# Kernel optimization log

Hardware: AMD Instinct MI355X
Metric: run time of the kernel (lower is better)

The kernel has to match this reference:

```python
import jax, jax.numpy as jnp
import numpy as np

NUM_EXPERTS = 8


def setup_inputs() -> dict:
    key = jax.random.key(0)
    k1, k2 = jax.random.split(key)
    G, T, D, E = 4, 2048, 1024, NUM_EXPERTS
    token_inputs = jax.random.normal(k1, (G, T, D), dtype=jnp.float32)
    router_weight = jax.random.normal(k2, (E, D), dtype=jnp.float32) * 0.02
    router_bias = jnp.zeros((E,), dtype=jnp.float32)
    return {
        "token_inputs": token_inputs,
        "router_weight": router_weight,
        "router_bias": router_bias,
        "expert_capacity": 320,
    }


def _routing(probs, expert_capacities):
    """Experts-preferred assignment: experts pick tokens in order, each up to
    its capacity, from tokens not yet taken by earlier experts."""
    G, T, E = probs.shape
    max_cap = max(expert_capacities)
    dispatch = jnp.zeros((G, T, E, max_cap), dtype=jnp.int32)
    combine = jnp.zeros((G, T, E, max_cap), dtype=probs.dtype)
    available = jnp.ones((G, T), dtype=probs.dtype)  # 1 if token unassigned
    g_idx = jnp.arange(G)[:, None]
    for e, cap in enumerate(expert_capacities):  # static small loop over experts
        masked = probs[:, :, e] * available                 # [G, T]
        gate, idx = jax.lax.top_k(masked, cap)              # [G, cap]
        c_idx = jnp.arange(cap)[None, :]
        dispatch = dispatch.at[g_idx, idx, e, c_idx].set(1)
        combine = combine.at[g_idx, idx, e, c_idx].set(gate)
        available = available.at[g_idx, idx].set(0.0)       # chosen tokens now taken
    return dispatch, combine


def reference(token_inputs, router_weight, router_bias, expert_capacity):
    x = token_inputs.astype(jnp.float32)
    # router logits: [G, T, E]
    logits = jnp.einsum("gtd,ed->gte", x, router_weight) + router_bias
    probs = jax.nn.softmax(logits, axis=-1)
    capacities = [int(expert_capacity)] * NUM_EXPERTS
    dispatch_mask, combine_array = _routing(probs, capacities)
    # router z-loss: mean over groups*tokens of logsumexp(logits)^2
    log_z = jax.nn.logsumexp(logits, axis=-1)
    z_loss = jnp.sum(log_z ** 2) / (logits.shape[0] * logits.shape[1])
    auxiliary_loss = jnp.float32(0.0)
    router_causal_loss = jnp.float32(0.0)
    return dispatch_mask, combine_array, auxiliary_loss, z_loss, router_causal_loss
```

## Files before the change

kernel.cpp:

```cpp
#include <hip/hip_runtime.h>

#define NEXP 8
typedef unsigned long long u64;
typedef unsigned int u32;

__global__ __launch_bounds__(512) void probs_fill_kernel(
    const float* __restrict__ x,
    const float* __restrict__ w,
    const float* __restrict__ bias,
    float* __restrict__ probsT,
    double* __restrict__ zpart,
    float* __restrict__ out,
    long long nout4,
    long long GT, int npb, int nfb)
{
    if ((int)blockIdx.x >= npb) {
        const int fb = (int)blockIdx.x - npb;
        const long long stride = (long long)nfb * 512;
        const float4 z = make_float4(0.f, 0.f, 0.f, 0.f);
        for (long long k = (long long)fb * 512 + threadIdx.x; k < nout4; k += stride) {
            reinterpret_cast<float4*>(out)[k] = z;
        }
        return;
    }

    __shared__ float wl[NEXP * 1024];
    __shared__ double zred[8];
    for (int i = threadIdx.x; i < NEXP * 1024 / 4; i += 512) {
        reinterpret_cast<float4*>(wl)[i] = reinterpret_cast<const float4*>(w)[i];
    }
    __syncthreads();

    const int wave = threadIdx.x >> 6;
    const int lane = threadIdx.x & 63;
    const long long t = (long long)blockIdx.x * 8 + wave;
    const float* xr = x + t * 1024;

    float acc[NEXP];
#pragma unroll
    for (int e = 0; e < NEXP; ++e) acc[e] = 0.f;

#pragma unroll
    for (int c = 0; c < 4; ++c) {
        const int d = c * 256 + lane * 4;
        const float4 xv = *reinterpret_cast<const float4*>(xr + d);
#pragma unroll
        for (int e = 0; e < NEXP; ++e) {
            const float4 wv = *reinterpret_cast<const float4*>(wl + e * 1024 + d);
            acc[e] = fmaf(xv.x, wv.x, acc[e]);
            acc[e] = fmaf(xv.y, wv.y, acc[e]);
            acc[e] = fmaf(xv.z, wv.z, acc[e]);
            acc[e] = fmaf(xv.w, wv.w, acc[e]);
        }
    }
#pragma unroll
    for (int e = 0; e < NEXP; ++e) {
#pragma unroll
        for (int off = 32; off; off >>= 1) acc[e] += __shfl_xor(acc[e], off, 64);
    }

    if (lane == 0) {
        double l[NEXP];
        double mx = -1e300;
#pragma unroll
        for (int e = 0; e < NEXP; ++e) {
            l[e] = (double)acc[e] + (double)bias[e];
            mx = fmax(mx, l[e]);
        }
        double ex[NEXP];
        double s = 0.0;
#pragma unroll
        for (int e = 0; e < NEXP; ++e) { ex[e] = exp(l[e] - mx); s += ex[e]; }
        const double inv = 1.0 / s;
#pragma unroll
        for (int e = 0; e < NEXP; ++e) probsT[(long long)e * GT + t] = (float)(ex[e] * inv);
        const double lse = mx + log(s);
        zred[wave] = lse * lse;
    }
    __syncthreads();
    if (threadIdx.x == 0) {
        double s = 0.0;
#pragma unroll
        for (int i = 0; i < 8; ++i) s += zred[i];
        zpart[blockIdx.x] = s;
    }
}

__global__ __launch_bounds__(256) void ranksort_kernel(
    const float* __restrict__ probsT,
    u64* __restrict__ skey,
    int T, int G, long long GT)
{
    __shared__ u64 keys[2048];
    const int nsub = T / 256;
    const int pair = blockIdx.x / nsub;
    const int sub  = blockIdx.x % nsub;
    const int e = pair / G;
    const int g = pair % G;
    const float* p = probsT + (long long)e * GT + (long long)g * T;

    for (int j = threadIdx.x; j < T; j += 256) {
        keys[j] = ((u64)__float_as_uint(p[j]) << 32) | (u32)(~(u32)j);
    }
    __syncthreads();

    const int i = sub * 256 + threadIdx.x;
    const u64 ki = keys[i];
    int r = 0;
    const ulonglong2* k2 = reinterpret_cast<const ulonglong2*>(keys);
#pragma unroll 8
    for (int j = 0; j < T / 2; ++j) {
        const ulonglong2 q = k2[j];
        r += (q.x > ki);
        r += (q.y > ki);
    }
    skey[(long long)pair * T + r] = ki;
}

__global__ __launch_bounds__(1024) void assign_kernel(
    const u64* __restrict__ skey,
    const double* __restrict__ zpart,
    int nzpart,
    float* __restrict__ out,
    int T, int G, int cap, long long GT)
{
    const int g = blockIdx.x;
    const int tid = threadIdx.x;
    const int lane = tid & 63;
    const int w = tid >> 6;

    __shared__ int avail[2048];
    __shared__ int cnt[32];
    __shared__ int off[32];
    __shared__ int totS;

    avail[tid] = 1;
    avail[tid + 1024] = 1;

    float* dispatch = out;
    float* combine  = out + GT * (long long)NEXP * cap;
    const long long gbase = (long long)g * T;
    const u64 lmask = (lane == 0) ? 0ull : ((~0ull) >> (64 - lane));

    for (int e = 0; e < NEXP; ++e) {
        __syncthreads();
        const long long kb = (long long)(e * G + g) * T;
        const u64 k0 = skey[kb + tid];
        const u64 k1 = skey[kb + tid + 1024];
        const u32 idx0 = ~(u32)k0;
        const u32 idx1 = ~(u32)k1;
        const float v0 = __uint_as_float((u32)(k0 >> 32));
        const float v1 = __uint_as_float((u32)(k1 >> 32));
        const int f0 = avail[idx0];
        const int f1 = avail[idx1];
        const u64 m0 = __ballot(f0);
        const u64 m1 = __ballot(f1);
        if (lane == 0) { cnt[w] = __popcll(m0); cnt[16 + w] = __popcll(m1); }
        __syncthreads();
        if (w == 0) {
            int v = (lane < 32) ? cnt[lane] : 0;
#pragma unroll
            for (int o = 1; o < 32; o <<= 1) { int t2 = __shfl_up(v, o, 64); if (lane >= o) v += t2; }
            if (lane < 32) off[lane] = v - cnt[lane];
            if (lane == 31) totS = v;
        }
        __syncthreads();
        const int S = totS;
        const int pre0 = off[w] + __popcll(m0 & lmask);
        const int pre1 = off[16 + w] + __popcll(m1 & lmask);
        const bool s0 = f0 && pre0 < cap;
        const bool s1 = f1 && pre1 < cap;
        if (s0) {
            const long long o_ = ((gbase + idx0) * NEXP + e) * (long long)cap + pre0;
            dispatch[o_] = 1.0f;
            combine[o_]  = v0;
        }
        if (s1) {
            const long long o_ = ((gbase + idx1) * NEXP + e) * (long long)cap + pre1;
            dispatch[o_] = 1.0f;
            combine[o_]  = v1;
        }
        if (S < cap) {
            const int u0 = 1 - avail[tid];
            const int u1 = 1 - avail[tid + 1024];
            const u64 n0 = __ballot(u0);
            const u64 n1 = __ballot(u1);
            if (lane == 0) { cnt[w] = __popcll(n0); cnt[16 + w] = __popcll(n1); }
            __syncthreads();
            if (w == 0) {
                int v = (lane < 32) ? cnt[lane] : 0;
#pragma unroll
                for (int o = 1; o < 32; o <<= 1) { int t2 = __shfl_up(v, o, 64); if (lane >= o) v += t2; }
                if (lane < 32) off[lane] = v - cnt[lane];
            }
            __syncthreads();
            const int q0 = off[w] + __popcll(n0 & lmask);
            const int q1 = off[16 + w] + __popcll(n1 & lmask);
            const int nfill = cap - S;
            if (u0 && q0 < nfill) {
                const long long o_ = ((gbase + tid) * NEXP + e) * (long long)cap + S + q0;
                dispatch[o_] = 1.0f;
            }
            if (u1 && q1 < nfill) {
                const long long o_ = ((gbase + tid + 1024) * NEXP + e) * (long long)cap + S + q1;
                dispatch[o_] = 1.0f;
            }
            __syncthreads();
        }
        if (s0) avail[idx0] = 0;
        if (s1) avail[idx1] = 0;
    }

    if (g == 0 && tid < 64) {
        double s = 0.0;
        for (int i = tid; i < nzpart; i += 64) s += zpart[i];
#pragma unroll
        for (int o = 32; o; o >>= 1) {
            s += __shfl_xor(s, o, 64);
        }
        if (tid == 0) {
            float* sc = out + 2 * GT * (long long)NEXP * cap;
            sc[0] = 0.0f;
            sc[1] = (float)(s / (double)GT);
            sc[2] = 0.0f;
        }
    }
}

extern "C" void kernel_launch(void* const* d_in, const int* in_sizes, int n_in,
                              void* d_out, int out_size, void* d_ws, size_t ws_size,
                              hipStream_t stream) {
    (void)n_in; (void)ws_size;
    const float* x    = (const float*)d_in[0];
    const float* w    = (const float*)d_in[1];
    const float* bias = (const float*)d_in[2];

    const int E = in_sizes[2];
    const int D = in_sizes[1] / E;
    const long long GT = (long long)in_sizes[0] / D;
    const int T = 2048;
    const int G = (int)(GT / T);
    const int cap = (int)(((long long)out_size - 3) / (2 * GT * E));
    const int npb = (int)(GT / 8);
    const int nfb = 2048;

    double* zpart = (double*)d_ws;
    float* probsT = (float*)((char*)d_ws + 16384);
    u64*   skey   = (u64*)((char*)d_ws + 16384 + (size_t)E * GT * sizeof(float));

    const long long nout4 = ((long long)out_size - 3) >> 2;

    probs_fill_kernel<<<npb + nfb, 512, 0, stream>>>(
        x, w, bias, probsT, zpart, (float*)d_out, nout4, GT, npb, nfb);

    ranksort_kernel<<<E * G * (T / 256), 256, 0, stream>>>(probsT, skey, T, G, GT);

    assign_kernel<<<G, 1024, 0, stream>>>(skey, zpart, npb, (float*)d_out, T, G, cap, GT);
}
```

Before: 80.13 us.

## Fuse router, rank sort and assignment into one persistent kernel with grid barriers

Merges the three kernels (probs+zero fill, rank sort, assignment) into a single 256-block persistent kernel that uses atomic-counter grid barriers between phases. Each block now handles 32 tokens, and the rank sort splits the comparison over 4 thread groups with a shared-memory reduction. The assignment phase preloads all sorted keys into registers and replaces the shared-memory prefix scans with per-wave shuffle scans, dropping several syncthreads per expert. The goal is to remove launch gaps and inter-kernel drains. In exchange it relies on all 256 blocks being co-resident and on a memset of the barrier counters, and runs fewer blocks for the zero fill and the projection.

```diff
diff --git a/kernel.cpp b/kernel.cpp
--- a/kernel.cpp
+++ b/kernel.cpp
@@ -1,141 +1,156 @@
 #include <hip/hip_runtime.h>
 
 #define NEXP 8
+#define NBLK 256
+#define NTHR 1024
+
 typedef unsigned long long u64;
 typedef unsigned int u32;
 
-__global__ __launch_bounds__(512) void probs_fill_kernel(
+union __align__(16) Smem {
+    struct { float wl[NEXP * 1024]; double zred[16]; } a;
+    struct { u64 keys[2048]; int part[NTHR]; } b;
+    struct { int avail[2048]; int cnt[32]; int cnt2[32]; } c;
+};
+
+__global__ __launch_bounds__(NTHR, 4) void moe_router_kernel(
     const float* __restrict__ x,
     const float* __restrict__ w,
     const float* __restrict__ bias,
+    float* __restrict__ out,
     float* __restrict__ probsT,
+    u64* __restrict__ skey,
     double* __restrict__ zpart,
-    float* __restrict__ out,
-    long long nout4,
-    long long GT, int npb, int nfb)
+    int* __restrict__ bar,
+    long long nout4, long long GT, int T, int G, int cap)
 {
-    if ((int)blockIdx.x >= npb) {
-        const int fb = (int)blockIdx.x - npb;
-        const long long stride = (long long)nfb * 512;
-        const float4 z = make_float4(0.f, 0.f, 0.f, 0.f);
-        for (long long k = (long long)fb * 512 + threadIdx.x; k < nout4; k += stride) {
-            reinterpret_cast<float4*>(out)[k] = z;
-        }
-        return;
-    }
-
-    __shared__ float wl[NEXP * 1024];
-    __shared__ double zred[8];
-    for (int i = threadIdx.x; i < NEXP * 1024 / 4; i += 512) {
-        reinterpret_cast<float4*>(wl)[i] = reinterpret_cast<const float4*>(w)[i];
-    }
-    __syncthreads();
-
-    const int wave = threadIdx.x >> 6;
-    const int lane = threadIdx.x & 63;
-    const long long t = (long long)blockIdx.x * 8 + wave;
-    const float* xr = x + t * 1024;
-
-    float acc[NEXP];
-#pragma unroll
-    for (int e = 0; e < NEXP; ++e) acc[e] = 0.f;
-
-#pragma unroll
-    for (int c = 0; c < 4; ++c) {
-        const int d = c * 256 + lane * 4;
-        const float4 xv = *reinterpret_cast<const float4*>(xr + d);
-#pragma unroll
-        for (int e = 0; e < NEXP; ++e) {
-            const float4 wv = *reinterpret_cast<const float4*>(wl + e * 1024 + d);
-            acc[e] = fmaf(xv.x, wv.x, acc[e]);
-            acc[e] = fmaf(xv.y, wv.y, acc[e]);
-            acc[e] = fmaf(xv.z, wv.z, acc[e]);
-            acc[e] = fmaf(xv.w, wv.w, acc[e]);
-        }
-    }
-#pragma unroll
-    for (int e = 0; e < NEXP; ++e) {
-#pragma unroll
-        for (int off = 32; off; off >>= 1) acc[e] += __shfl_xor(acc[e], off, 64);
-    }
-
-    if (lane == 0) {
-        double l[NEXP];
-        double mx = -1e300;
-#pragma unroll
-        for (int e = 0; e < NEXP; ++e) {
-            l[e] = (double)acc[e] + (double)bias[e];
-            mx = fmax(mx, l[e]);
-        }
-        double ex[NEXP];
-        double s = 0.0;
-#pragma unroll
-        for (int e = 0; e < NEXP; ++e) { ex[e] = exp(l[e] - mx); s += ex[e]; }
-        const double inv = 1.0 / s;
-#pragma unroll
-        for (int e = 0; e < NEXP; ++e) probsT[(long long)e * GT + t] = (float)(ex[e] * inv);
-        const double lse = mx + log(s);
-        zred[wave] = lse * lse;
-    }
-    __syncthreads();
-    if (threadIdx.x == 0) {
-        double s = 0.0;
-#pragma unroll
-        for (int i = 0; i < 8; ++i) s += zred[i];
-        zpart[blockIdx.x] = s;
-    }
-}
-
-__global__ __launch_bounds__(256) void ranksort_kernel(
-    const float* __restrict__ probsT,
-    u64* __restrict__ skey,
-    int T, int G, long long GT)
-{
-    __shared__ u64 keys[2048];
-    const int nsub = T / 256;
-    const int pair = blockIdx.x / nsub;
-    const int sub  = blockIdx.x % nsub;
-    const int e = pair / G;
-    const int g = pair % G;
-    const float* p = probsT + (long long)e * GT + (long long)g * T;
-
-    for (int j = threadIdx.x; j < T; j += 256) {
-        keys[j] = ((u64)__float_as_uint(p[j]) << 32) | (u32)(~(u32)j);
-    }
-    __syncthreads();
-
-    const int i = sub * 256 + threadIdx.x;
-    const u64 ki = keys[i];
-    int r = 0;
-    const ulonglong2* k2 = reinterpret_cast<const ulonglong2*>(keys);
-#pragma unroll 8
-    for (int j = 0; j < T / 2; ++j) {
-        const ulonglong2 q = k2[j];
-        r += (q.x > ki);
-        r += (q.y > ki);
-    }
-    skey[(long long)pair * T + r] = ki;
-}
-
-__global__ __launch_bounds__(1024) void assign_kernel(
-    const u64* __restrict__ skey,
-    const double* __restrict__ zpart,
-    int nzpart,
-    float* __restrict__ out,
-    int T, int G, int cap, long long GT)
-{
-    const int g = blockIdx.x;
+    __shared__ Smem sm;
+    const int b = blockIdx.x;
     const int tid = threadIdx.x;
     const int lane = tid & 63;
-    const int w = tid >> 6;
-
-    __shared__ int avail[2048];
-    __shared__ int cnt[32];
-    __shared__ int off[32];
-    __shared__ int totS;
-
-    avail[tid] = 1;
-    avail[tid + 1024] = 1;
+    const int wv = tid >> 6;
+
+    for (int i = tid; i < NEXP * 1024 / 4; i += NTHR)
+        reinterpret_cast<float4*>(sm.a.wl)[i] = reinterpret_cast<const float4*>(w)[i];
+    __syncthreads();
+
+    {
+        const float4 z = make_float4(0.f, 0.f, 0.f, 0.f);
+        for (long long k = (long long)b * NTHR + tid; k < nout4; k += (long long)NBLK * NTHR)
+            reinterpret_cast<float4*>(out)[k] = z;
+    }
+
+    {
+        double zacc = 0.0;
+#pragma unroll
+        for (int s = 0; s < 2; ++s) {
+            const long long t = (long long)b * 32 + wv * 2 + s;
+            const float* xr = x + t * 1024;
+            float acc[NEXP];
+#pragma unroll
+            for (int e = 0; e < NEXP; ++e) acc[e] = 0.f;
+#pragma unroll
+            for (int c = 0; c < 4; ++c) {
+                const float4 xv = reinterpret_cast<const float4*>(xr)[c * 64 + lane];
+#pragma unroll
+                for (int e = 0; e < NEXP; ++e) {
+                    const float4 wv4 = reinterpret_cast<const float4*>(sm.a.wl + e * 1024)[c * 64 + lane];
+                    acc[e] = fmaf(xv.x, wv4.x, acc[e]);
+                    acc[e] = fmaf(xv.y, wv4.y, acc[e]);
+                    acc[e] = fmaf(xv.z, wv4.z, acc[e]);
+                    acc[e] = fmaf(xv.w, wv4.w, acc[e]);
+                }
+            }
+#pragma unroll
+            for (int e = 0; e < NEXP; ++e) {
+#pragma unroll
+                for (int off = 32; off; off >>= 1) acc[e] += __shfl_xor(acc[e], off, 64);
+            }
+            if (lane == 0) {
+                double l[NEXP]; double mx = -1e300;
+#pragma unroll
+                for (int e = 0; e < NEXP; ++e) { l[e] = (double)acc[e] + (double)bias[e]; mx = fmax(mx, l[e]); }
+                double ex[NEXP]; double ssum = 0.0;
+#pragma unroll
+                for (int e = 0; e < NEXP; ++e) { ex[e] = exp(l[e] - mx); ssum += ex[e]; }
+                const double inv = 1.0 / ssum;
+#pragma unroll
+                for (int e = 0; e < NEXP; ++e) probsT[(long long)e * GT + t] = (float)(ex[e] * inv);
+                const double lse = mx + log(ssum);
+                zacc += lse * lse;
+            }
+        }
+        if (lane == 0) sm.a.zred[wv] = zacc;
+    }
+    __syncthreads();
+    if (tid == 0) {
+        double s = 0.0;
+#pragma unroll
+        for (int i = 0; i < 16; ++i) s += sm.a.zred[i];
+        zpart[b] = s;
+    }
+
+    __syncthreads();
+    if (tid == 0) {
+        __threadfence();
+        atomicAdd(&bar[0], 1);
+        while (__hip_atomic_load(&bar[0], __ATOMIC_RELAXED, __HIP_MEMORY_SCOPE_AGENT) < NBLK)
+            __builtin_amdgcn_s_sleep(2);
+        __threadfence();
+    }
+    __syncthreads();
+
+    {
+        const int pair = b >> 3;
+        const int sub  = b & 7;
+        const int e = pair / G;
+        const int g = pair - e * G;
+        const float* p = probsT + (long long)e * GT + (long long)g * T;
+        for (int j = tid; j < 2048; j += NTHR)
+            sm.b.keys[j] = ((u64)__float_as_uint(p[j]) << 32) | (u32)(~(u32)j);
+        __syncthreads();
+        const int slot = tid & 255;
+        const int q = tid >> 8;
+        const u64 kt = sm.b.keys[sub * 256 + slot];
+        const ulonglong2* k2 = reinterpret_cast<const ulonglong2*>(sm.b.keys) + q * 256;
+        int r = 0;
+#pragma unroll 8
+        for (int j = 0; j < 256; ++j) {
+            const ulonglong2 v = k2[j];
+            r += (v.x > kt); r += (v.y > kt);
+        }
+        sm.b.part[tid] = r;
+        __syncthreads();
+        if (tid < 256) {
+            const int rank = sm.b.part[tid] + sm.b.part[tid + 256] + sm.b.part[tid + 512] + sm.b.part[tid + 768];
+            skey[(long long)pair * T + rank] = sm.b.keys[sub * 256 + tid];
+        }
+    }
+
+    __syncthreads();
+    if (b >= G) {
+        if (tid == 0) { __threadfence(); atomicAdd(&bar[1], 1); }
+        return;
+    }
+    if (tid == 0) {
+        __threadfence();
+        atomicAdd(&bar[1], 1);
+        while (__hip_atomic_load(&bar[1], __ATOMIC_RELAXED, __HIP_MEMORY_SCOPE_AGENT) < NBLK)
+            __builtin_amdgcn_s_sleep(2);
+        __threadfence();
+    }
+    __syncthreads();
+
+    const int g = b;
+    u64 ka[NEXP], kb[NEXP];
+#pragma unroll
+    for (int e = 0; e < NEXP; ++e) {
+        const long long base = (long long)(e * G + g) * T;
+        ka[e] = skey[base + tid];
+        kb[e] = skey[base + tid + 1024];
+    }
+    sm.c.avail[tid] = 1;
+    sm.c.avail[tid + 1024] = 1;
 
     float* dispatch = out;
     float* combine  = out + GT * (long long)NEXP * cap;
@@ -144,80 +159,54 @@
 
     for (int e = 0; e < NEXP; ++e) {
         __syncthreads();
-        const long long kb = (long long)(e * G + g) * T;
-        const u64 k0 = skey[kb + tid];
-        const u64 k1 = skey[kb + tid + 1024];
-        const u32 idx0 = ~(u32)k0;
-        const u32 idx1 = ~(u32)k1;
+        const u64 k0 = ka[e], k1 = kb[e];
+        const u32 idx0 = ~(u32)k0, idx1 = ~(u32)k1;
         const float v0 = __uint_as_float((u32)(k0 >> 32));
         const float v1 = __uint_as_float((u32)(k1 >> 32));
-        const int f0 = avail[idx0];
-        const int f1 = avail[idx1];
+        const int f0 = sm.c.avail[idx0];
+        const int f1 = sm.c.avail[idx1];
         const u64 m0 = __ballot(f0);
         const u64 m1 = __ballot(f1);
-        if (lane == 0) { cnt[w] = __popcll(m0); cnt[16 + w] = __popcll(m1); }
-        __syncthreads();
-        if (w == 0) {
-            int v = (lane < 32) ? cnt[lane] : 0;
-#pragma unroll
-            for (int o = 1; o < 32; o <<= 1) { int t2 = __shfl_up(v, o, 64); if (lane >= o) v += t2; }
-            if (lane < 32) off[lane] = v - cnt[lane];
-            if (lane == 31) totS = v;
-        }
-        __syncthreads();
-        const int S = totS;
-        const int pre0 = off[w] + __popcll(m0 & lmask);
-        const int pre1 = off[16 + w] + __popcll(m1 & lmask);
-        const bool s0 = f0 && pre0 < cap;
-        const bool s1 = f1 && pre1 < cap;
-        if (s0) {
-            const long long o_ = ((gbase + idx0) * NEXP + e) * (long long)cap + pre0;
-            dispatch[o_] = 1.0f;
-            combine[o_]  = v0;
-        }
-        if (s1) {
-            const long long o_ = ((gbase + idx1) * NEXP + e) * (long long)cap + pre1;
-            dispatch[o_] = 1.0f;
-            combine[o_]  = v1;
-        }
+        if (lane == 0) { sm.c.cnt[wv] = __popcll(m0); sm.c.cnt[16 + wv] = __popcll(m1); }
+        __syncthreads();
+        int vi = (lane < 32) ? sm.c.cnt[lane] : 0;
+#pragma unroll
+        for (int o = 1; o < 32; o <<= 1) { const int t2 = __shfl_up(vi, o, 64); if (lane >= o) vi += t2; }
+        const int off0 = wv ? __shfl(vi, wv - 1, 64) : 0;
+        const int off1 = __shfl(vi, 15 + wv, 64);
+        const int S    = __shfl(vi, 31, 64);
+        const int pre0 = off0 + __popcll(m0 & lmask);
+        const int pre1 = off1 + __popcll(m1 & lmask);
+        const bool s0 = f0 && (pre0 < cap);
+        const bool s1 = f1 && (pre1 < cap);
+        if (s0) { const long long o_ = ((gbase + idx0) * NEXP + e) * (long long)cap + pre0; dispatch[o_] = 1.0f; combine[o_] = v0; }
+        if (s1) { const long long o_ = ((gbase + idx1) * NEXP + e) * (long long)cap + pre1; dispatch[o_] = 1.0f; combine[o_] = v1; }
         if (S < cap) {
-            const int u0 = 1 - avail[tid];
-            const int u1 = 1 - avail[tid + 1024];
+            const int u0 = 1 - sm.c.avail[tid];
+            const int u1 = 1 - sm.c.avail[tid + 1024];
             const u64 n0 = __ballot(u0);
             const u64 n1 = __ballot(u1);
-            if (lane == 0) { cnt[w] = __popcll(n0); cnt[16 + w] = __popcll(n1); }
+            if (lane == 0) { sm.c.cnt2[wv] = __popcll(n0); sm.c.cnt2[16 + wv] = __popcll(n1); }
             __syncthreads();
-            if (w == 0) {
-                int v = (lane < 32) ? cnt[lane] : 0;
-#pragma unroll
-                for (int o = 1; o < 32; o <<= 1) { int t2 = __shfl_up(v, o, 64); if (lane >= o) v += t2; }
-                if (lane < 32) off[lane] = v - cnt[lane];
-            }
-            __syncthreads();
-            const int q0 = off[w] + __popcll(n0 & lmask);
-            const int q1 = off[16 + w] + __popcll(n1 & lmask);
+            int vj = (lane < 32) ? sm.c.cnt2[lane] : 0;
+#pragma unroll
+            for (int o = 1; o < 32; o <<= 1) { const int t2 = __shfl_up(vj, o, 64); if (lane >= o) vj += t2; }
+            const int qoff0 = wv ? __shfl(vj, wv - 1, 64) : 0;
+            const int qoff1 = __shfl(vj, 15 + wv, 64);
+            const int q0 = qoff0 + __popcll(n0 & lmask);
+            const int q1 = qoff1 + __popcll(n1 & lmask);
             const int nfill = cap - S;
-            if (u0 && q0 < nfill) {
-                const long long o_ = ((gbase + tid) * NEXP + e) * (long long)cap + S + q0;
-                dispatch[o_] = 1.0f;
-            }
-            if (u1 && q1 < nfill) {
-                const long long o_ = ((gbase + tid + 1024) * NEXP + e) * (long long)cap + S + q1;
-                dispatch[o_] = 1.0f;
-            }
-            __syncthreads();
-        }
-        if (s0) avail[idx0] = 0;
-        if (s1) avail[idx1] = 0;
+            if (u0 && q0 < nfill) { const long long o_ = ((gbase + tid) * NEXP + e) * (long long)cap + S + q0; dispatch[o_] = 1.0f; }
+            if (u1 && q1 < nfill) { const long long o_ = ((gbase + tid + 1024) * NEXP + e) * (long long)cap + S + q1; dispatch[o_] = 1.0f; }
+        }
+        if (s0) sm.c.avail[idx0] = 0;
+        if (s1) sm.c.avail[idx1] = 0;
     }
 
     if (g == 0 && tid < 64) {
-        double s = 0.0;
-        for (int i = tid; i < nzpart; i += 64) s += zpart[i];
-#pragma unroll
-        for (int o = 32; o; o >>= 1) {
-            s += __shfl_xor(s, o, 64);
-        }
+        double s = zpart[tid] + zpart[tid + 64] + zpart[tid + 128] + zpart[tid + 192];
+#pragma unroll
+        for (int o = 32; o; o >>= 1) s += __shfl_xor(s, o, 64);
         if (tid == 0) {
             float* sc = out + 2 * GT * (long long)NEXP * cap;
             sc[0] = 0.0f;
@@ -241,19 +230,16 @@
     const int T = 2048;
     const int G = (int)(GT / T);
     const int cap = (int)(((long long)out_size - 3) / (2 * GT * E));
-    const int npb = (int)(GT / 8);
-    const int nfb = 2048;
-
-    double* zpart = (double*)d_ws;
-    float* probsT = (float*)((char*)d_ws + 16384);
-    u64*   skey   = (u64*)((char*)d_ws + 16384 + (size_t)E * GT * sizeof(float));
-
     const long long nout4 = ((long long)out_size - 3) >> 2;
 
-    probs_fill_kernel<<<npb + nfb, 512, 0, stream>>>(
-        x, w, bias, probsT, zpart, (float*)d_out, nout4, GT, npb, nfb);
-
-    ranksort_kernel<<<E * G * (T / 256), 256, 0, stream>>>(probsT, skey, T, G, GT);
-
-    assign_kernel<<<G, 1024, 0, stream>>>(skey, zpart, npb, (float*)d_out, T, G, cap, GT);
+    int*    bar    = (int*)d_ws;
+    double* zpart  = (double*)((char*)d_ws + 4096);
+    float*  probsT = (float*)((char*)d_ws + 16384);
+    u64*    skey   = (u64*)((char*)d_ws + 16384 + (size_t)E * GT * sizeof(float));
+
+    hipMemsetAsync(bar, 0, 16, stream);
+
+    moe_router_kernel<<<NBLK, NTHR, 0, stream>>>(
+        x, w, bias, (float*)d_out, probsT, skey, zpart, bar,
+        nout4, GT, T, G, cap);
 }
```

Result: slower. 87.62 us (+9.3%).
